# Optimization experiments

Hardware: AMD Instinct MI355X
Metric: run time of the kernel (lower is better)

## Reference

```python
import jax, jax.numpy as jnp
import numpy as np

EPS_DIST = 1e-10
BN_EPS = 1e-5
K = 3


def setup_inputs() -> dict:
    key = jax.random.key(0)
    ks = jax.random.split(key, 8)
    B, N1, N2, C1, C2 = 16, 4096, 1024, 128, 256
    inp = {
        "xyz1": jax.random.normal(ks[0], (B, N1, 3), jnp.float32),
        "xyz2": jax.random.normal(ks[1], (B, N2, 3), jnp.float32),
        "points1": jax.random.normal(ks[2], (B, C1, N1), jnp.float32),
        "points2": jax.random.normal(ks[3], (B, C2, N2), jnp.float32),
        "W0": jax.random.normal(ks[4], (256, C1 + C2), jnp.float32) * 0.05,
        "b0": jax.random.normal(ks[5], (256,), jnp.float32) * 0.05,
        "g0": jnp.ones((256,), jnp.float32),
        "be0": jnp.zeros((256,), jnp.float32),
        "W1": jax.random.normal(ks[6], (128, 256), jnp.float32) * 0.05,
        "b1": jax.random.normal(ks[7], (128,), jnp.float32) * 0.05,
        "g1": jnp.ones((128,), jnp.float32),
        "be1": jnp.zeros((128,), jnp.float32),
    }
    return inp


def _conv_bn_relu(x, W, b, g, beta):
    # 1x1 Conv1d == channel matmul; BN in training mode (biased batch stats over B,N)
    x = jnp.einsum("oc,bcn->bon", W, x) + b[None, :, None]
    m = jnp.mean(x, axis=(0, 2), keepdims=True)
    v = jnp.var(x, axis=(0, 2), keepdims=True)
    x = g[None, :, None] * (x - m) * jax.lax.rsqrt(v + BN_EPS) + beta[None, :, None]
    return jax.nn.relu(x)


def reference(xyz1, xyz2, points1, points2, W0, b0, g0, be0, W1, b1, g1, be1):
    B, N1, _ = xyz1.shape
    # squared pairwise distances [B, N1, N2]
    d = (
        jnp.sum(xyz1 ** 2, -1)[:, :, None]
        + jnp.sum(xyz2 ** 2, -1)[:, None, :]
        - 2.0 * jnp.einsum("bnd,bmd->bnm", xyz1, xyz2)
    )
    d = jnp.maximum(d, EPS_DIST)
    neg, idx = jax.lax.top_k(-d, K)  # smallest K
    dist = -neg  # [B, N1, K]
    w = 1.0 / dist
    w = w / jnp.sum(w, axis=-1, keepdims=True)
    # gather neighbor features: [B, N1, K, C2]
    gathered = points2[jnp.arange(B)[:, None, None], :, idx]
    interp = jnp.einsum("bnkc,bnk->bcn", gathered, w)  # [B, C2, N1]
    x = jnp.concatenate([points1, interp], axis=1)  # [B, C1+C2, N1]
    x = _conv_bn_relu(x, W0, b0, g0, be0)
    x = _conv_bn_relu(x, W1, b1, g1, be1)
    return x
```

## Files before the change

### kernel.cpp

```cpp
#include <hip/hip_runtime.h>

#define EPS_DIST 1e-10f
#define BN_EPS 1e-5f

typedef short short8 __attribute__((ext_vector_type(8)));
typedef float floatx4 __attribute__((ext_vector_type(4)));

__device__ __forceinline__ unsigned short f2bf(float f) {
  unsigned u = __float_as_uint(f);
  unsigned r = (u + 0x7FFFu + ((u >> 16) & 1u)) >> 16;
  return (unsigned short)r;
}
__device__ __forceinline__ float bf2f(unsigned short h) {
  return __uint_as_float(((unsigned)h) << 16);
}

__device__ __forceinline__ void gload16(const void* g, void* l) {
  __builtin_amdgcn_global_load_lds(
      (const __attribute__((address_space(1))) unsigned int*)g,
      (__attribute__((address_space(3))) unsigned int*)l, 16, 0, 0);
}

__global__ __launch_bounds__(256) void tcvtw_kernel(
    const float* __restrict__ src, unsigned short* __restrict__ dst,
    const float* __restrict__ W0, const float* __restrict__ W1,
    unsigned short* __restrict__ Wb) {
  const int tid = threadIdx.x;
  if (blockIdx.z == 16) {
    int blk = blockIdx.y * 16 + blockIdx.x;
    int base = blk * 2048 + tid;
#pragma unroll
    for (int p = 0; p < 8; ++p) {
      int i = base + p * 256;
      float v = (i < 98304) ? W0[i] : W1[i - 98304];
      Wb[i] = f2bf(v);
    }
    return;
  }
  const int K = 256, N = 1024;
  __shared__ float sm[64][65];
  const int n0 = blockIdx.x * 64, k0 = blockIdx.y * 64, b = blockIdx.z;
  const int nl = tid & 63, kq = tid >> 6;
  const float* s = src + ((size_t)b * K + k0) * N + n0;
#pragma unroll
  for (int p = 0; p < 16; ++p) {
    int kl = p * 4 + kq;
    sm[kl][nl] = s[(size_t)kl * N + nl];
  }
  __syncthreads();
#pragma unroll
  for (int p = 0; p < 2; ++p) {
    int c = p * 256 + tid;
    int rn = c >> 3, jj = c & 7;
    short8 v;
#pragma unroll
    for (int u = 0; u < 8; ++u) v[u] = (short)f2bf(sm[jj * 8 + u][rn]);
    *(short8*)(dst + (size_t)(b * N + n0 + rn) * K + k0 + jj * 8) = v;
  }
}

__global__ __launch_bounds__(256) void tcvt_kernel(
    const float* __restrict__ src, unsigned short* __restrict__ dst,
    int K, int N) {
  __shared__ float sm[64][65];
  const int n0 = blockIdx.x * 64, k0 = blockIdx.y * 64, b = blockIdx.z;
  const int tid = threadIdx.x;
  const int nl = tid & 63, kq = tid >> 6;
  const float* s = src + ((size_t)b * K + k0) * N + n0;
#pragma unroll
  for (int p = 0; p < 16; ++p) {
    int kl = p * 4 + kq;
    sm[kl][nl] = s[(size_t)kl * N + nl];
  }
  __syncthreads();
#pragma unroll
  for (int p = 0; p < 2; ++p) {
    int c = p * 256 + tid;
    int rn = c >> 3, jj = c & 7;
    short8 v;
#pragma unroll
    for (int u = 0; u < 8; ++u) v[u] = (short)f2bf(sm[jj * 8 + u][rn]);
    *(short8*)(dst + (size_t)(b * N + n0 + rn) * K + k0 + jj * 8) = v;
  }
}

__global__ __launch_bounds__(256) void zgemm_kernel(
    const unsigned short* __restrict__ Wb, const unsigned short* __restrict__ Xt2,
    unsigned short* __restrict__ Zt) {
  __shared__ short sA[2][64 * 32];
  __shared__ short sB[2][128 * 32];
  const int lin = blockIdx.x;
  const int xcd = lin & 7;
  const int slot = lin >> 3;
  const int b = xcd * 2 + (slot >> 5);
  const int inner = slot & 31;
  const int o0 = (inner & 3) * 64;
  const int m0 = (inner >> 2) * 128;
  const int tid = threadIdx.x, lane = tid & 63, w = tid >> 6;
  const int wo = w >> 1, wn = w & 1, quad = lane >> 4, l15 = lane & 15;
  const int c0 = tid, c1 = 256 + tid;
  const int rA = tid >> 2, jA = tid & 3;
  const int r0 = c0 >> 2, j0 = c0 & 3, r1 = c1 >> 2, j1 = c1 & 3;
  const unsigned short* x2b = Xt2 + (size_t)b * 1024 * 256;
  auto STAGE = [&](int h, int kb) {
    gload16(Wb + (size_t)(o0 + rA) * 384 + 128 + kb + jA * 8, &sA[h][tid * 8]);
    gload16(x2b + (size_t)(m0 + r0) * 256 + kb + j0 * 8, &sB[h][c0 * 8]);
    gload16(x2b + (size_t)(m0 + r1) * 256 + kb + j1 * 8, &sB[h][c1 * 8]);
  };
  floatx4 acc[2][4] = {};
  STAGE(0, 0);
  asm volatile("s_waitcnt vmcnt(0)" ::: "memory");
  __syncthreads();
  int cur = 0;
  for (int t = 0; t < 8; ++t) {
    if (t < 7) STAGE(cur ^ 1, (t + 1) * 32);
    short8 av[2], bv[4];
#pragma unroll
    for (int i = 0; i < 2; ++i)
      av[i] = *(const short8*)(&sA[cur][(wo * 32 + i * 16 + l15) * 32 + quad * 8]);
#pragma unroll
    for (int j = 0; j < 4; ++j)
      bv[j] = *(const short8*)(&sB[cur][(wn * 64 + j * 16 + l15) * 32 + quad * 8]);
#pragma unroll
    for (int i = 0; i < 2; ++i)
#pragma unroll
      for (int j = 0; j < 4; ++j)
        acc[i][j] = __builtin_amdgcn_mfma_f32_16x16x32_bf16(av[i], bv[j], acc[i][j], 0, 0, 0);
    if (t < 7) {
      asm volatile("s_waitcnt vmcnt(0)" ::: "memory");
      __syncthreads();
      cur ^= 1;
    }
  }
#pragma unroll
  for (int i = 0; i < 2; ++i) {
    int ob = o0 + wo * 32 + i * 16 + quad * 4;
#pragma unroll
    for (int j = 0; j < 4; ++j) {
      int m = m0 + wn * 64 + j * 16 + l15;
      ushort4 out;
      out.x = f2bf(acc[i][j][0]); out.y = f2bf(acc[i][j][1]);
      out.z = f2bf(acc[i][j][2]); out.w = f2bf(acc[i][j][3]);
      *(ushort4*)(Zt + (size_t)(b * 1024 + m) * 256 + ob) = out;
    }
  }
}

__global__ __launch_bounds__(256) void knni_kernel(
    const float* __restrict__ xyz1, const float* __restrict__ xyz2,
    const unsigned short* __restrict__ Zt, unsigned short* __restrict__ y0t) {
  __shared__ float4 s2[1024];
  __shared__ int sidx[96];
  __shared__ float swgt[96];
  const int lin = blockIdx.x;
  const int xcd = lin & 7;
  const int slot = lin >> 3;
  const int b = xcd * 2 + (slot >> 7);
  const int qtile = slot & 127;
  const int tid = threadIdx.x;
  const float* x2 = xyz2 + b * 3072;
  for (int j = tid; j < 1024; j += 256) {
    float x = x2[j * 3 + 0], y = x2[j * 3 + 1], z = x2[j * 3 + 2];
    s2[j] = make_float4(x, y, z, (x * x + y * y) + z * z);
  }
  __syncthreads();
  const int q = tid >> 3, sub = tid & 7;
  const int n = qtile * 32 + q;
  const float* p1 = xyz1 + (b * 4096 + n) * 3;
  const float ax = p1[0], ay = p1[1], az = p1[2];
  const float s1 = (ax * ax + ay * ay) + az * az;
  float d0 = 3.4e38f, d1 = 3.4e38f, d2 = 3.4e38f;
  int i0 = 0x7fffffff, i1 = 0x7fffffff, i2 = 0x7fffffff;
  for (int jj = 0; jj < 128; ++jj) {
    int j = jj * 8 + sub;
    float4 c = s2[j];
    float dot = (ax * c.x + ay * c.y) + az * c.z;
    float d = fmaxf((s1 + c.w) - 2.0f * dot, EPS_DIST);
    bool lt0 = d < d0, lt1 = d < d1, lt2 = d < d2;
    d2 = lt1 ? d1 : (lt2 ? d : d2);
    i2 = lt1 ? i1 : (lt2 ? j : i2);
    d1 = lt0 ? d0 : (lt1 ? d : d1);
    i1 = lt0 ? i0 : (lt1 ? j : i1);
    d0 = lt0 ? d : d0;
    i0 = lt0 ? j : i0;
  }
#pragma unroll
  for (int m = 1; m <= 4; m <<= 1) {
    float e0 = __shfl_xor(d0, m), e1 = __shfl_xor(d1, m), e2 = __shfl_xor(d2, m);
    int   f0 = __shfl_xor(i0, m), f1 = __shfl_xor(i1, m), f2 = __shfl_xor(i2, m);
    float A[3] = {d0, d1, d2}, Bv[3] = {e0, e1, e2};
    int   I[3] = {i0, i1, i2}, J[3] = {f0, f1, f2};
    float md[3]; int mi[3];
    int pa = 0, pb = 0;
#pragma unroll
    for (int k = 0; k < 3; ++k) {
      float da = A[pa], db = Bv[pb];
      int ia = I[pa], ib = J[pb];
      bool ta = (da < db) || (da == db && ia < ib);
      md[k] = ta ? da : db; mi[k] = ta ? ia : ib;
      pa += ta ? 1 : 0; pb += ta ? 0 : 1;
    }
    d0 = md[0]; d1 = md[1]; d2 = md[2];
    i0 = mi[0]; i1 = mi[1]; i2 = mi[2];
  }
  if (sub == 0) {
    float w0 = 1.0f / d0, w1 = 1.0f / d1, w2 = 1.0f / d2;
    float s = (w0 + w1) + w2;
    sidx[q * 3 + 0] = i0; sidx[q * 3 + 1] = i1; sidx[q * 3 + 2] = i2;
    swgt[q * 3 + 0] = w0 / s; swgt[q * 3 + 1] = w1 / s; swgt[q * 3 + 2] = w2 / s;
  }
  __syncthreads();
  const int w = tid >> 6, lane = tid & 63;
  const unsigned short* zb = Zt + (size_t)b * 1024 * 256;
#pragma unroll
  for (int t = 0; t < 8; ++t) {
    int nl = w * 8 + t;
    int nn = qtile * 32 + nl;
    int g0 = sidx[nl * 3 + 0], g1 = sidx[nl * 3 + 1], g2 = sidx[nl * 3 + 2];
    float w0 = swgt[nl * 3 + 0], w1 = swgt[nl * 3 + 1], w2 = swgt[nl * 3 + 2];
    ushort4 r0 = *(const ushort4*)(zb + (size_t)g0 * 256 + lane * 4);
    ushort4 r1 = *(const ushort4*)(zb + (size_t)g1 * 256 + lane * 4);
    ushort4 r2 = *(const ushort4*)(zb + (size_t)g2 * 256 + lane * 4);
    ushort4 o;
    o.x = f2bf(w0 * bf2f(r0.x) + w1 * bf2f(r1.x) + w2 * bf2f(r2.x));
    o.y = f2bf(w0 * bf2f(r0.y) + w1 * bf2f(r1.y) + w2 * bf2f(r2.y));
    o.z = f2bf(w0 * bf2f(r0.z) + w1 * bf2f(r1.z) + w2 * bf2f(r2.z));
    o.w = f2bf(w0 * bf2f(r0.w) + w1 * bf2f(r1.w) + w2 * bf2f(r2.w));
    *(ushort4*)(y0t + ((size_t)b * 4096 + nn) * 256 + lane * 4) = o;
  }
}

__global__ __launch_bounds__(256) void gemm0_kernel(
    const unsigned short* __restrict__ Wb, const unsigned short* __restrict__ Xt1,
    const float* __restrict__ b0,
    unsigned short* __restrict__ y0t, float* __restrict__ acc0) {
  __shared__ short sA[2][128 * 32];
  __shared__ short sB[2][128 * 32];
  __shared__ float ls[256];
  const int lin = blockIdx.x;
  const int xcd = lin & 7;
  const int slot = lin >> 3;
  const int b = xcd * 2 + (slot >> 6);
  const int inner = slot & 63;
  const int o0 = (inner & 1) * 128;
  const int n0 = (inner >> 1) * 128;
  const int tid = threadIdx.x, lane = tid & 63, w = tid >> 6;
  const int wo = w >> 1, wn = w & 1, quad = lane >> 4, l15 = lane & 15;
  const int c0 = tid, c1 = 256 + tid;
  const int r0 = c0 >> 2, j0 = c0 & 3, r1 = c1 >> 2, j1 = c1 & 3;
  const unsigned short* xb = Xt1 + (size_t)(b * 4096 + n0) * 128;
  ls[tid] = 0.f;
  auto STAGE = [&](int h, int kb) {
    gload16(Wb + (size_t)(o0 + r0) * 384 + kb + j0 * 8, &sA[h][c0 * 8]);
    gload16(Wb + (size_t)(o0 + r1) * 384 + kb + j1 * 8, &sA[h][c1 * 8]);
    gload16(xb + (size_t)r0 * 128 + kb + j0 * 8, &sB[h][c0 * 8]);
    gload16(xb + (size_t)r1 * 128 + kb + j1 * 8, &sB[h][c1 * 8]);
  };
  floatx4 acc[4][4] = {};
  STAGE(0, 0);
  asm volatile("s_waitcnt vmcnt(0)" ::: "memory");
  __syncthreads();
  int cur = 0;
  for (int t = 0; t < 4; ++t) {
    if (t < 3) STAGE(cur ^ 1, (t + 1) * 32);
    short8 av[4], bv[4];
#pragma unroll
    for (int i = 0; i < 4; ++i)
      av[i] = *(const short8*)(&sA[cur][(wo * 64 + i * 16 + l15) * 32 + quad * 8]);
#pragma unroll
    for (int j = 0; j < 4; ++j)
      bv[j] = *(const short8*)(&sB[cur][(wn * 64 + j * 16 + l15) * 32 + quad * 8]);
#pragma unroll
    for (int i = 0; i < 4; ++i)
#pragma unroll
      for (int j = 0; j < 4; ++j)
        acc[i][j] = __builtin_amdgcn_mfma_f32_16x16x32_bf16(av[i], bv[j], acc[i][j], 0, 0, 0);
    if (t < 3) {
      asm volatile("s_waitcnt vmcnt(0)" ::: "memory");
      __syncthreads();
      cur ^= 1;
    }
  }
#pragma unroll
  for (int i = 0; i < 4; ++i) {
    int obg = o0 + wo * 64 + i * 16 + quad * 4;
    floatx4 bias = *(const floatx4*)(b0 + obg);
    float ps[4] = {0.f, 0.f, 0.f, 0.f}, pq[4] = {0.f, 0.f, 0.f, 0.f};
#pragma unroll
    for (int j = 0; j < 4; ++j) {
      int n = n0 + wn * 64 + j * 16 + l15;
      unsigned short* yp = y0t + (size_t)(b * 4096 + n) * 256 + obg;
      ushort4 zr = *(const ushort4*)yp;
      ushort4 out;
      float v0 = acc[i][j][0] + bf2f(zr.x) + bias[0];
      float v1 = acc[i][j][1] + bf2f(zr.y) + bias[1];
      float v2 = acc[i][j][2] + bf2f(zr.z) + bias[2];
      float v3 = acc[i][j][3] + bf2f(zr.w) + bias[3];
      out.x = f2bf(v0); out.y = f2bf(v1); out.z = f2bf(v2); out.w = f2bf(v3);
      *(ushort4*)yp = out;
      float q0 = bf2f(out.x), q1 = bf2f(out.y), q2 = bf2f(out.z), q3 = bf2f(out.w);
      ps[0] += q0; ps[1] += q1; ps[2] += q2; ps[3] += q3;
      pq[0] += q0 * q0; pq[1] += q1 * q1; pq[2] += q2 * q2; pq[3] += q3 * q3;
    }
    int lo = obg - o0;
#pragma unroll
    for (int uu = 0; uu < 4; ++uu) {
      int u = (l15 + uu) & 3;
      atomicAdd(&ls[lo + u], ps[u]);
      atomicAdd(&ls[128 + lo + u], pq[u]);
    }
  }
  __syncthreads();
  if (tid < 128) {
    atomicAdd(&acc0[o0 + tid], ls[tid]);
    atomicAdd(&acc0[256 + o0 + tid], ls[128 + tid]);
  }
}

__global__ __launch_bounds__(256) void gemm1_kernel(
    const unsigned short* __restrict__ Wb, const unsigned short* __restrict__ y0t,
    const float* __restrict__ acc0, const float* __restrict__ g0,
    const float* __restrict__ be0, const float* __restrict__ b1,
    float* __restrict__ y1, float* __restrict__ acc1) {
  __shared__ short sA[2][128 * 32];
  __shared__ short sB[2][128 * 32];
  __shared__ float sst[512];
  __shared__ float ls[256];
  const int lin = blockIdx.x;
  const int xcd = lin & 7;
  const int slot = lin >> 3;
  const int b = xcd * 2 + (slot >> 5);
  const int n0 = (slot & 31) * 128;
  const int tid = threadIdx.x, lane = tid & 63, w = tid >> 6;
  const int wm = w & 1, wo2 = w >> 1, quad = lane >> 4, l15 = lane & 15;
  const unsigned short* W1b = Wb + 98304;
  const int c0 = tid, c1 = 256 + tid;
  const int r0 = c0 >> 2, j0 = c0 & 3, r1 = c1 >> 2, j1 = c1 & 3;
  const unsigned short* yb = y0t + (size_t)(b * 4096 + n0) * 256;
  short8 ra0, ra1;
  auto LOADRAW = [&](int kb) {
    ra0 = *(const short8*)(yb + (size_t)r0 * 256 + kb + j0 * 8);
    ra1 = *(const short8*)(yb + (size_t)r1 * 256 + kb + j1 * 8);
  };
  auto XFORM = [&](int h, int kb) {
    int k0b = kb + j0 * 8, k1b = kb + j1 * 8;
    short8 v0, v1;
#pragma unroll
    for (int u = 0; u < 8; ++u) {
      float t0 = fmaxf(bf2f((unsigned short)ra0[u]) * sst[k0b + u] + sst[256 + k0b + u], 0.f);
      float t1 = fmaxf(bf2f((unsigned short)ra1[u]) * sst[k1b + u] + sst[256 + k1b + u], 0.f);
      v0[u] = (short)f2bf(t0);
      v1[u] = (short)f2bf(t1);
    }
    *(short8*)(&sA[h][c0 * 8]) = v0;
    *(short8*)(&sA[h][c1 * 8]) = v1;
  };
  auto STAGEB = [&](int h, int kb) {
    gload16(W1b + (size_t)r0 * 256 + kb + j0 * 8, &sB[h][c0 * 8]);
    gload16(W1b + (size_t)r1 * 256 + kb + j1 * 8, &sB[h][c1 * 8]);
  };
  LOADRAW(0);
  {
    const float inv = 1.0f / 65536.0f;
    float mean = acc0[tid] * inv;
    float var = acc0[256 + tid] * inv - mean * mean;
    float sc = g0[tid] / sqrtf(var + BN_EPS);
    sst[tid] = sc;
    sst[256 + tid] = be0[tid] - mean * sc;
  }
  ls[tid] = 0.f;
  __syncthreads();
  XFORM(0, 0);
  STAGEB(0, 0);
  asm volatile("s_waitcnt vmcnt(0)" ::: "memory");
  __syncthreads();
  floatx4 acc[4][4] = {};
  int cur = 0;
  for (int t = 0; t < 8; ++t) {
    if (t < 7) {
      LOADRAW((t + 1) * 32);
      STAGEB(cur ^ 1, (t + 1) * 32);
    }
    short8 av[4], bv[4];
#pragma unroll
    for (int i = 0; i < 4; ++i)
      av[i] = *(const short8*)(&sA[cur][(wm * 64 + i * 16 + l15) * 32 + quad * 8]);
#pragma unroll
    for (int j = 0; j < 4; ++j)
      bv[j] = *(const short8*)(&sB[cur][(wo2 * 64 + j * 16 + l15) * 32 + quad * 8]);
#pragma unroll
    for (int i = 0; i < 4; ++i)
#pragma unroll
      for (int j = 0; j < 4; ++j)
        acc[i][j] = __builtin_amdgcn_mfma_f32_16x16x32_bf16(av[i], bv[j], acc[i][j], 0, 0, 0);
    if (t < 7) {
      XFORM(cur ^ 1, (t + 1) * 32);
      asm volatile("s_waitcnt vmcnt(0)" ::: "memory");
      __syncthreads();
      cur ^= 1;
    }
  }
#pragma unroll
  for (int j = 0; j < 4; ++j) {
    int o = wo2 * 64 + j * 16 + l15;
    float bias = b1[o];
    float s = 0.f, q = 0.f;
#pragma unroll
    for (int i = 0; i < 4; ++i) {
      int n = n0 + wm * 64 + i * 16 + quad * 4;
      floatx4 v = acc[i][j] + bias;
      *(floatx4*)(y1 + (size_t)(b * 128 + o) * 4096 + n) = v;
      s += (v[0] + v[1]) + (v[2] + v[3]);
      q += (v[0] * v[0] + v[1] * v[1]) + (v[2] * v[2] + v[3] * v[3]);
    }
    s += __shfl_xor(s, 16); s += __shfl_xor(s, 32);
    q += __shfl_xor(q, 16); q += __shfl_xor(q, 32);
    if (quad == 0) {
      atomicAdd(&ls[o], s);
      atomicAdd(&ls[128 + o], q);
    }
  }
  __syncthreads();
  if (tid < 128) {
    atomicAdd(&acc1[tid], ls[tid]);
    atomicAdd(&acc1[128 + tid], ls[128 + tid]);
  }
}

__global__ __launch_bounds__(256) void bnrelu_f_kernel(
    float* __restrict__ y, const float* __restrict__ acc1,
    const float* __restrict__ g1, const float* __restrict__ be1) {
  size_t i4 = (size_t)blockIdx.x * 256 + threadIdx.x;
  int o = (int)((i4 * 4) >> 12) & 127;
  const float inv = 1.0f / 65536.0f;
  float m = acc1[o] * inv;
  float var = acc1[128 + o] * inv - m * m;
  float sc = g1[o] / sqrtf(var + BN_EPS);
  float bb = be1[o];
  floatx4 v = ((floatx4*)y)[i4];
  floatx4 r;
  r[0] = fmaxf((v[0] - m) * sc + bb, 0.f);
  r[1] = fmaxf((v[1] - m) * sc + bb, 0.f);
  r[2] = fmaxf((v[2] - m) * sc + bb, 0.f);
  r[3] = fmaxf((v[3] - m) * sc + bb, 0.f);
  ((floatx4*)y)[i4] = r;
}

extern "C" void kernel_launch(void* const* d_in, const int* in_sizes, int n_in,
                              void* d_out, int out_size, void* d_ws, size_t ws_size,
                              hipStream_t stream) {
  (void)in_sizes; (void)n_in; (void)out_size; (void)ws_size;
  const float* xyz1    = (const float*)d_in[0];
  const float* xyz2    = (const float*)d_in[1];
  const float* points1 = (const float*)d_in[2];
  const float* points2 = (const float*)d_in[3];
  const float* W0  = (const float*)d_in[4];
  const float* b0  = (const float*)d_in[5];
  const float* g0  = (const float*)d_in[6];
  const float* be0 = (const float*)d_in[7];
  const float* W1  = (const float*)d_in[8];
  const float* b1  = (const float*)d_in[9];
  const float* g1  = (const float*)d_in[10];
  const float* be1 = (const float*)d_in[11];

  char* ws = (char*)d_ws;
  float* acc0 = (float*)(ws + 1576960);
  float* acc1 = (float*)(ws + 1579008);
  unsigned short* Wb  = (unsigned short*)(ws + 1581056);
  unsigned short* Xt2 = (unsigned short*)(ws + 2097152);
  unsigned short* Xt1 = (unsigned short*)(ws + 10485760);
  unsigned short* y0t = (unsigned short*)(ws + 27262976);
  unsigned short* Zt = (unsigned short*)d_out;
  float* y1 = (float*)d_out;

  hipMemsetAsync(acc0, 0, 3072, stream);
  tcvtw_kernel<<<dim3(16, 4, 17), 256, 0, stream>>>(points2, Xt2, W0, W1, Wb);
  tcvt_kernel<<<dim3(64, 2, 16), 256, 0, stream>>>(points1, Xt1, 128, 4096);
  zgemm_kernel<<<512, 256, 0, stream>>>(Wb, Xt2, Zt);
  knni_kernel<<<2048, 256, 0, stream>>>(xyz1, xyz2, Zt, y0t);
  gemm0_kernel<<<1024, 256, 0, stream>>>(Wb, Xt1, b0, y0t, acc0);
  gemm1_kernel<<<512, 256, 0, stream>>>(Wb, y0t, acc0, g0, be0, b1, y1, acc1);
  bnrelu_f_kernel<<<8192, 256, 0, stream>>>(y1, acc1, g1, be1);
}
```

Baseline: 265.7 us.

## Interpolate raw features then run full-K gemm0; merge convert kernels; per-XCD stats

```diff
diff --git a/kernel.cpp b/kernel.cpp
--- a/kernel.cpp
+++ b/kernel.cpp
@@ -21,14 +21,15 @@
       (__attribute__((address_space(3))) unsigned int*)l, 16, 0, 0);
 }
 
-__global__ __launch_bounds__(256) void tcvtw_kernel(
-    const float* __restrict__ src, unsigned short* __restrict__ dst,
+__global__ __launch_bounds__(256) void tcvt_all_kernel(
+    const float* __restrict__ p2, unsigned short* __restrict__ Xt2,
+    const float* __restrict__ p1, unsigned short* __restrict__ Xt1,
     const float* __restrict__ W0, const float* __restrict__ W1,
     unsigned short* __restrict__ Wb) {
   const int tid = threadIdx.x;
-  if (blockIdx.z == 16) {
-    int blk = blockIdx.y * 16 + blockIdx.x;
-    int base = blk * 2048 + tid;
+  const int id = blockIdx.x;
+  if (id >= 3072) {
+    int base = (id - 3072) * 2048 + tid;
 #pragma unroll
     for (int p = 0; p < 8; ++p) {
       int i = base + p * 256;
@@ -37,9 +38,16 @@
     }
     return;
   }
-  const int K = 256, N = 1024;
   __shared__ float sm[64][65];
-  const int n0 = blockIdx.x * 64, k0 = blockIdx.y * 64, b = blockIdx.z;
+  const float* src; unsigned short* dst; int K, N, n0, k0, b;
+  if (id < 1024) {
+    src = p2; dst = Xt2; K = 256; N = 1024;
+    n0 = (id & 15) * 64; k0 = ((id >> 4) & 3) * 64; b = id >> 6;
+  } else {
+    int q = id - 1024;
+    src = p1; dst = Xt1; K = 128; N = 4096;
+    n0 = (q & 63) * 64; k0 = ((q >> 6) & 1) * 64; b = q >> 7;
+  }
   const int nl = tid & 63, kq = tid >> 6;
   const float* s = src + ((size_t)b * K + k0) * N + n0;
 #pragma unroll
@@ -59,96 +67,9 @@
   }
 }
 
-__global__ __launch_bounds__(256) void tcvt_kernel(
-    const float* __restrict__ src, unsigned short* __restrict__ dst,
-    int K, int N) {
-  __shared__ float sm[64][65];
-  const int n0 = blockIdx.x * 64, k0 = blockIdx.y * 64, b = blockIdx.z;
-  const int tid = threadIdx.x;
-  const int nl = tid & 63, kq = tid >> 6;
-  const float* s = src + ((size_t)b * K + k0) * N + n0;
-#pragma unroll
-  for (int p = 0; p < 16; ++p) {
-    int kl = p * 4 + kq;
-    sm[kl][nl] = s[(size_t)kl * N + nl];
-  }
-  __syncthreads();
-#pragma unroll
-  for (int p = 0; p < 2; ++p) {
-    int c = p * 256 + tid;
-    int rn = c >> 3, jj = c & 7;
-    short8 v;
-#pragma unroll
-    for (int u = 0; u < 8; ++u) v[u] = (short)f2bf(sm[jj * 8 + u][rn]);
-    *(short8*)(dst + (size_t)(b * N + n0 + rn) * K + k0 + jj * 8) = v;
-  }
-}
-
-__global__ __launch_bounds__(256) void zgemm_kernel(
-    const unsigned short* __restrict__ Wb, const unsigned short* __restrict__ Xt2,
-    unsigned short* __restrict__ Zt) {
-  __shared__ short sA[2][64 * 32];
-  __shared__ short sB[2][128 * 32];
-  const int lin = blockIdx.x;
-  const int xcd = lin & 7;
-  const int slot = lin >> 3;
-  const int b = xcd * 2 + (slot >> 5);
-  const int inner = slot & 31;
-  const int o0 = (inner & 3) * 64;
-  const int m0 = (inner >> 2) * 128;
-  const int tid = threadIdx.x, lane = tid & 63, w = tid >> 6;
-  const int wo = w >> 1, wn = w & 1, quad = lane >> 4, l15 = lane & 15;
-  const int c0 = tid, c1 = 256 + tid;
-  const int rA = tid >> 2, jA = tid & 3;
-  const int r0 = c0 >> 2, j0 = c0 & 3, r1 = c1 >> 2, j1 = c1 & 3;
-  const unsigned short* x2b = Xt2 + (size_t)b * 1024 * 256;
-  auto STAGE = [&](int h, int kb) {
-    gload16(Wb + (size_t)(o0 + rA) * 384 + 128 + kb + jA * 8, &sA[h][tid * 8]);
-    gload16(x2b + (size_t)(m0 + r0) * 256 + kb + j0 * 8, &sB[h][c0 * 8]);
-    gload16(x2b + (size_t)(m0 + r1) * 256 + kb + j1 * 8, &sB[h][c1 * 8]);
-  };
-  floatx4 acc[2][4] = {};
-  STAGE(0, 0);
-  asm volatile("s_waitcnt vmcnt(0)" ::: "memory");
-  __syncthreads();
-  int cur = 0;
-  for (int t = 0; t < 8; ++t) {
-    if (t < 7) STAGE(cur ^ 1, (t + 1) * 32);
-    short8 av[2], bv[4];
-#pragma unroll
-    for (int i = 0; i < 2; ++i)
-      av[i] = *(const short8*)(&sA[cur][(wo * 32 + i * 16 + l15) * 32 + quad * 8]);
-#pragma unroll
-    for (int j = 0; j < 4; ++j)
-      bv[j] = *(const short8*)(&sB[cur][(wn * 64 + j * 16 + l15) * 32 + quad * 8]);
-#pragma unroll
-    for (int i = 0; i < 2; ++i)
-#pragma unroll
-      for (int j = 0; j < 4; ++j)
-        acc[i][j] = __builtin_amdgcn_mfma_f32_16x16x32_bf16(av[i], bv[j], acc[i][j], 0, 0, 0);
-    if (t < 7) {
-      asm volatile("s_waitcnt vmcnt(0)" ::: "memory");
-      __syncthreads();
-      cur ^= 1;
-    }
-  }
-#pragma unroll
-  for (int i = 0; i < 2; ++i) {
-    int ob = o0 + wo * 32 + i * 16 + quad * 4;
-#pragma unroll
-    for (int j = 0; j < 4; ++j) {
-      int m = m0 + wn * 64 + j * 16 + l15;
-      ushort4 out;
-      out.x = f2bf(acc[i][j][0]); out.y = f2bf(acc[i][j][1]);
-      out.z = f2bf(acc[i][j][2]); out.w = f2bf(acc[i][j][3]);
-      *(ushort4*)(Zt + (size_t)(b * 1024 + m) * 256 + ob) = out;
-    }
-  }
-}
-
 __global__ __launch_bounds__(256) void knni_kernel(
     const float* __restrict__ xyz1, const float* __restrict__ xyz2,
-    const unsigned short* __restrict__ Zt, unsigned short* __restrict__ y0t) {
+    const unsigned short* __restrict__ Xt2, unsigned short* __restrict__ Xi) {
   __shared__ float4 s2[1024];
   __shared__ int sidx[96];
   __shared__ float swgt[96];
@@ -211,7 +132,7 @@
   }
   __syncthreads();
   const int w = tid >> 6, lane = tid & 63;
-  const unsigned short* zb = Zt + (size_t)b * 1024 * 256;
+  const unsigned short* zb = Xt2 + (size_t)b * 1024 * 256;
 #pragma unroll
   for (int t = 0; t < 8; ++t) {
     int nl = w * 8 + t;
@@ -226,14 +147,14 @@
     o.y = f2bf(w0 * bf2f(r0.y) + w1 * bf2f(r1.y) + w2 * bf2f(r2.y));
     o.z = f2bf(w0 * bf2f(r0.z) + w1 * bf2f(r1.z) + w2 * bf2f(r2.z));
     o.w = f2bf(w0 * bf2f(r0.w) + w1 * bf2f(r1.w) + w2 * bf2f(r2.w));
-    *(ushort4*)(y0t + ((size_t)b * 4096 + nn) * 256 + lane * 4) = o;
+    *(ushort4*)(Xi + ((size_t)b * 4096 + nn) * 256 + lane * 4) = o;
   }
 }
 
 __global__ __launch_bounds__(256) void gemm0_kernel(
     const unsigned short* __restrict__ Wb, const unsigned short* __restrict__ Xt1,
-    const float* __restrict__ b0,
-    unsigned short* __restrict__ y0t, float* __restrict__ acc0) {
+    const unsigned short* __restrict__ Xi, const float* __restrict__ b0,
+    unsigned short* __restrict__ y0t, float* __restrict__ acc0x) {
   __shared__ short sA[2][128 * 32];
   __shared__ short sB[2][128 * 32];
   __shared__ float ls[256];
@@ -249,20 +170,26 @@
   const int c0 = tid, c1 = 256 + tid;
   const int r0 = c0 >> 2, j0 = c0 & 3, r1 = c1 >> 2, j1 = c1 & 3;
   const unsigned short* xb = Xt1 + (size_t)(b * 4096 + n0) * 128;
+  const unsigned short* xi = Xi + (size_t)(b * 4096 + n0) * 256;
   ls[tid] = 0.f;
   auto STAGE = [&](int h, int kb) {
     gload16(Wb + (size_t)(o0 + r0) * 384 + kb + j0 * 8, &sA[h][c0 * 8]);
     gload16(Wb + (size_t)(o0 + r1) * 384 + kb + j1 * 8, &sA[h][c1 * 8]);
-    gload16(xb + (size_t)r0 * 128 + kb + j0 * 8, &sB[h][c0 * 8]);
-    gload16(xb + (size_t)r1 * 128 + kb + j1 * 8, &sB[h][c1 * 8]);
+    if (kb < 128) {
+      gload16(xb + (size_t)r0 * 128 + kb + j0 * 8, &sB[h][c0 * 8]);
+      gload16(xb + (size_t)r1 * 128 + kb + j1 * 8, &sB[h][c1 * 8]);
+    } else {
+      gload16(xi + (size_t)r0 * 256 + (kb - 128) + j0 * 8, &sB[h][c0 * 8]);
+      gload16(xi + (size_t)r1 * 256 + (kb - 128) + j1 * 8, &sB[h][c1 * 8]);
+    }
   };
   floatx4 acc[4][4] = {};
   STAGE(0, 0);
   asm volatile("s_waitcnt vmcnt(0)" ::: "memory");
   __syncthreads();
   int cur = 0;
-  for (int t = 0; t < 4; ++t) {
-    if (t < 3) STAGE(cur ^ 1, (t + 1) * 32);
+  for (int t = 0; t < 12; ++t) {
+    if (t < 11) STAGE(cur ^ 1, (t + 1) * 32);
     short8 av[4], bv[4];
 #pragma unroll
     for (int i = 0; i < 4; ++i)
@@ -275,7 +202,7 @@
 #pragma unroll
       for (int j = 0; j < 4; ++j)
         acc[i][j] = __builtin_amdgcn_mfma_f32_16x16x32_bf16(av[i], bv[j], acc[i][j], 0, 0, 0);
-    if (t < 3) {
+    if (t < 11) {
       asm volatile("s_waitcnt vmcnt(0)" ::: "memory");
       __syncthreads();
       cur ^= 1;
@@ -289,39 +216,45 @@
 #pragma unroll
     for (int j = 0; j < 4; ++j) {
       int n = n0 + wn * 64 + j * 16 + l15;
-      unsigned short* yp = y0t + (size_t)(b * 4096 + n) * 256 + obg;
-      ushort4 zr = *(const ushort4*)yp;
       ushort4 out;
-      float v0 = acc[i][j][0] + bf2f(zr.x) + bias[0];
-      float v1 = acc[i][j][1] + bf2f(zr.y) + bias[1];
-      float v2 = acc[i][j][2] + bf2f(zr.z) + bias[2];
-      float v3 = acc[i][j][3] + bf2f(zr.w) + bias[3];
-      out.x = f2bf(v0); out.y = f2bf(v1); out.z = f2bf(v2); out.w = f2bf(v3);
-      *(ushort4*)yp = out;
+      out.x = f2bf(acc[i][j][0] + bias[0]);
+      out.y = f2bf(acc[i][j][1] + bias[1]);
+      out.z = f2bf(acc[i][j][2] + bias[2]);
+      out.w = f2bf(acc[i][j][3] + bias[3]);
+      *(ushort4*)(y0t + (size_t)(b * 4096 + n) * 256 + obg) = out;
       float q0 = bf2f(out.x), q1 = bf2f(out.y), q2 = bf2f(out.z), q3 = bf2f(out.w);
       ps[0] += q0; ps[1] += q1; ps[2] += q2; ps[3] += q3;
       pq[0] += q0 * q0; pq[1] += q1 * q1; pq[2] += q2 * q2; pq[3] += q3 * q3;
     }
-    int lo = obg - o0;
-#pragma unroll
-    for (int uu = 0; uu < 4; ++uu) {
-      int u = (l15 + uu) & 3;
-      atomicAdd(&ls[lo + u], ps[u]);
-      atomicAdd(&ls[128 + lo + u], pq[u]);
+#pragma unroll
+    for (int m = 1; m <= 8; m <<= 1) {
+#pragma unroll
+      for (int u = 0; u < 4; ++u) {
+        ps[u] += __shfl_xor(ps[u], m);
+        pq[u] += __shfl_xor(pq[u], m);
+      }
+    }
+    if (l15 == 0) {
+      int lo = obg - o0;
+#pragma unroll
+      for (int u = 0; u < 4; ++u) {
+        atomicAdd(&ls[lo + u], ps[u]);
+        atomicAdd(&ls[128 + lo + u], pq[u]);
+      }
     }
   }
   __syncthreads();
   if (tid < 128) {
-    atomicAdd(&acc0[o0 + tid], ls[tid]);
-    atomicAdd(&acc0[256 + o0 + tid], ls[128 + tid]);
+    atomicAdd(&acc0x[xcd * 512 + o0 + tid], ls[tid]);
+    atomicAdd(&acc0x[xcd * 512 + 256 + o0 + tid], ls[128 + tid]);
   }
 }
 
 __global__ __launch_bounds__(256) void gemm1_kernel(
     const unsigned short* __restrict__ Wb, const unsigned short* __restrict__ y0t,
-    const float* __restrict__ acc0, const float* __restrict__ g0,
+    const float* __restrict__ acc0x, const float* __restrict__ g0,
     const float* __restrict__ be0, const float* __restrict__ b1,
-    float* __restrict__ y1, float* __restrict__ acc1) {
+    float* __restrict__ y1, float* __restrict__ acc1x) {
   __shared__ short sA[2][128 * 32];
   __shared__ short sB[2][128 * 32];
   __shared__ float sst[512];
@@ -362,8 +295,14 @@
   LOADRAW(0);
   {
     const float inv = 1.0f / 65536.0f;
-    float mean = acc0[tid] * inv;
-    float var = acc0[256 + tid] * inv - mean * mean;
+    float s0 = 0.f, s1 = 0.f;
+#pragma unroll
+    for (int x = 0; x < 8; ++x) {
+      s0 += acc0x[x * 512 + tid];
+      s1 += acc0x[x * 512 + 256 + tid];
+    }
+    float mean = s0 * inv;
+    float var = s1 * inv - mean * mean;
     float sc = g0[tid] / sqrtf(var + BN_EPS);
     sst[tid] = sc;
     sst[256 + tid] = be0[tid] - mean * sc;
@@ -422,19 +361,25 @@
   }
   __syncthreads();
   if (tid < 128) {
-    atomicAdd(&acc1[tid], ls[tid]);
-    atomicAdd(&acc1[128 + tid], ls[128 + tid]);
+    atomicAdd(&acc1x[xcd * 256 + tid], ls[tid]);
+    atomicAdd(&acc1x[xcd * 256 + 128 + tid], ls[128 + tid]);
   }
 }
 
 __global__ __launch_bounds__(256) void bnrelu_f_kernel(
-    float* __restrict__ y, const float* __restrict__ acc1,
+    float* __restrict__ y, const float* __restrict__ acc1x,
     const float* __restrict__ g1, const float* __restrict__ be1) {
   size_t i4 = (size_t)blockIdx.x * 256 + threadIdx.x;
-  int o = (int)((i4 * 4) >> 12) & 127;
+  int o = (int)(blockIdx.x >> 2) & 127;
   const float inv = 1.0f / 65536.0f;
-  float m = acc1[o] * inv;
-  float var = acc1[128 + o] * inv - m * m;
+  float s0 = 0.f, s1 = 0.f;
+#pragma unroll
+  for (int x = 0; x < 8; ++x) {
+    s0 += acc1x[x * 256 + o];
+    s1 += acc1x[x * 256 + 128 + o];
+  }
+  float m = s0 * inv;
+  float var = s1 * inv - m * m;
   float sc = g1[o] / sqrtf(var + BN_EPS);
   float bb = be1[o];
   floatx4 v = ((floatx4*)y)[i4];
@@ -464,21 +409,19 @@
   const float* be1 = (const float*)d_in[11];
 
   char* ws = (char*)d_ws;
-  float* acc0 = (float*)(ws + 1576960);
-  float* acc1 = (float*)(ws + 1579008);
+  float* acc0x = (float*)(ws + 0);
+  float* acc1x = (float*)(ws + 16384);
   unsigned short* Wb  = (unsigned short*)(ws + 1581056);
   unsigned short* Xt2 = (unsigned short*)(ws + 2097152);
   unsigned short* Xt1 = (unsigned short*)(ws + 10485760);
   unsigned short* y0t = (unsigned short*)(ws + 27262976);
-  unsigned short* Zt = (unsigned short*)d_out;
+  unsigned short* Xi = (unsigned short*)d_out;
   float* y1 = (float*)d_out;
 
-  hipMemsetAsync(acc0, 0, 3072, stream);
-  tcvtw_kernel<<<dim3(16, 4, 17), 256, 0, stream>>>(points2, Xt2, W0, W1, Wb);
-  tcvt_kernel<<<dim3(64, 2, 16), 256, 0, stream>>>(points1, Xt1, 128, 4096);
-  zgemm_kernel<<<512, 256, 0, stream>>>(Wb, Xt2, Zt);
-  knni_kernel<<<2048, 256, 0, stream>>>(xyz1, xyz2, Zt, y0t);
-  gemm0_kernel<<<1024, 256, 0, stream>>>(Wb, Xt1, b0, y0t, acc0);
-  gemm1_kernel<<<512, 256, 0, stream>>>(Wb, y0t, acc0, g0, be0, b1, y1, acc1);
-  bnrelu_f_kernel<<<8192, 256, 0, stream>>>(y1, acc1, g1, be1);
-}
+  hipMemsetAsync(acc0x, 0, 24576, stream);
+  tcvt_all_kernel<<<3136, 256, 0, stream>>>(points2, Xt2, points1, Xt1, W0, W1, Wb);
+  knni_kernel<<<2048, 256, 0, stream>>>(xyz1, xyz2, Xt2, Xi);
+  gemm0_kernel<<<1024, 256, 0, stream>>>(Wb, Xt1, Xi, b0, y0t, acc0x);
+  gemm1_kernel<<<512, 256, 0, stream>>>(Wb, y0t, acc0x, g0, be0, b1, y1, acc1x);
+  bnrelu_f_kernel<<<8192, 256, 0, stream>>>(y1, acc1x, g1, be1);
+}
```

After: 225.2 us. -15.2%, faster.
